# Kernel optimization log

Measured on AMD Instinct MI355X. Metric: run time of the kernel, lower is better.

Reference implementation:

```python
import jax, jax.numpy as jnp
import numpy as np

N_HEAD = 16
LN_EPS = 1e-5


def _rope_tables(T, hd, dtype):
    # Standard GPT-NeoX style rotary tables: cos/sin of shape [T, hd]
    inv = 1.0 / (10000.0 ** (np.arange(0, hd, 2, dtype=np.float64) / hd))
    freqs = np.outer(np.arange(T), inv)
    emb = np.concatenate([freqs, freqs], axis=-1)
    return jnp.asarray(np.cos(emb), dtype), jnp.asarray(np.sin(emb), dtype)


def _rotate_half(x):
    x1, x2 = jnp.split(x, 2, axis=-1)
    return jnp.concatenate([-x2, x1], axis=-1)


def _layernorm(x, g, b):
    mu = x.mean(-1, keepdims=True)
    var = x.var(-1, keepdims=True)
    return (x - mu) / jnp.sqrt(var + LN_EPS) * g + b


def _heads(x, H):
    B, T, C = x.shape
    return x.reshape(B, T, H, C // H).transpose(0, 2, 1, 3)  # [B,H,T,hd]


def _lin_attention(Q, K, V, causal):
    # Q,K,V: [B,H,T,hd]; ELU+1 feature map, RoPE on features, denom = sum_s Q.K
    Qf = jax.nn.elu(Q) + 1.0
    Kf = jax.nn.elu(K) + 1.0
    hd = Qf.shape[-1]
    cq, sq = _rope_tables(Qf.shape[2], hd, Qf.dtype)
    ck, sk = _rope_tables(Kf.shape[2], hd, Kf.dtype)
    Qr = Qf * cq + _rotate_half(Qf) * sq
    Kr = Kf * ck + _rotate_half(Kf) * sk
    # denom.sum(-1) == Qf . (sum_s Kf) -- avoid materializing a second TxS matrix
    denom = jnp.einsum('bhtd,bhd->bht', Qf, Kf.sum(axis=2))[..., None]
    att = jnp.einsum('bhtd,bhsd->bhts', Qr, Kr)
    if causal:
        T, S = att.shape[-2], att.shape[-1]
        att = jnp.where(jnp.tril(jnp.ones((T, S), dtype=bool)), att, 0.0)
    att = att / denom
    y = jnp.einsum('bhts,bhsd->bhtd', att, V)
    B, H, T, hd = y.shape
    return y.transpose(0, 2, 1, 3).reshape(B, T, H * hd)


def _forward(x, memory, ln1_g, ln1_b, sa_qkv_w, sa_qkv_b, sa_proj_w, sa_proj_b,
             ln2_g, ln2_b, ca_q_w, ca_q_b, ca_kv_w, ca_kv_b, ca_proj_w, ca_proj_b,
             ln3_g, ln3_b, fc_w, fc_b, fcp_w, fcp_b):
    H = N_HEAD
    # causal self-attention
    h = _layernorm(x, ln1_g, ln1_b)
    qkv = h @ sa_qkv_w + sa_qkv_b
    Q, K, V = jnp.split(qkv, 3, axis=-1)
    y = _lin_attention(_heads(Q, H), _heads(K, H), _heads(V, H), causal=True)
    x = x + (y @ sa_proj_w + sa_proj_b)
    # cross-attention
    h = _layernorm(x, ln2_g, ln2_b)
    q = h @ ca_q_w + ca_q_b
    kv = memory @ ca_kv_w + ca_kv_b
    K, V = jnp.split(kv, 2, axis=-1)
    y = _lin_attention(_heads(q, H), _heads(K, H), _heads(V, H), causal=False)
    x = x + (y @ ca_proj_w + ca_proj_b)
    # MLP with tanh-approx GELU
    h = _layernorm(x, ln3_g, ln3_b)
    h = jax.nn.gelu(h @ fc_w + fc_b, approximate=True)
    x = x + (h @ fcp_w + fcp_b)
    return x


def setup_inputs() -> dict:
    key = jax.random.key(0)
    ks = jax.random.split(key, 12)
    B, T, S, C = 2, 1024, 1024, 1024
    w = lambda k, shape: jax.random.normal(k, shape, dtype=jnp.float32) * 0.02
    return {
        'x': jax.random.normal(ks[0], (B, T, C), dtype=jnp.float32),
        'memory': jax.random.normal(ks[1], (B, S, C), dtype=jnp.float32),
        'ln1_g': jnp.ones((C,), jnp.float32), 'ln1_b': jnp.zeros((C,), jnp.float32),
        'sa_qkv_w': w(ks[2], (C, 3 * C)), 'sa_qkv_b': jnp.zeros((3 * C,), jnp.float32),
        'sa_proj_w': w(ks[3], (C, C)), 'sa_proj_b': jnp.zeros((C,), jnp.float32),
        'ln2_g': jnp.ones((C,), jnp.float32), 'ln2_b': jnp.zeros((C,), jnp.float32),
        'ca_q_w': w(ks[4], (C, C)), 'ca_q_b': jnp.zeros((C,), jnp.float32),
        'ca_kv_w': w(ks[5], (C, 2 * C)), 'ca_kv_b': jnp.zeros((2 * C,), jnp.float32),
        'ca_proj_w': w(ks[6], (C, C)), 'ca_proj_b': jnp.zeros((C,), jnp.float32),
        'ln3_g': jnp.ones((C,), jnp.float32), 'ln3_b': jnp.zeros((C,), jnp.float32),
        'fc_w': w(ks[7], (C, 4 * C)), 'fc_b': jnp.zeros((4 * C,), jnp.float32),
        'fcp_w': w(ks[8], (4 * C, C)), 'fcp_b': jnp.zeros((C,), jnp.float32),
    }


def reference(x, memory, ln1_g, ln1_b, sa_qkv_w, sa_qkv_b, sa_proj_w, sa_proj_b,
              ln2_g, ln2_b, ca_q_w, ca_q_b, ca_kv_w, ca_kv_b, ca_proj_w, ca_proj_b,
              ln3_g, ln3_b, fc_w, fc_b, fcp_w, fcp_b):
    return _forward(x, memory, ln1_g, ln1_b, sa_qkv_w, sa_qkv_b, sa_proj_w, sa_proj_b,
                    ln2_g, ln2_b, ca_q_w, ca_q_b, ca_kv_w, ca_kv_b, ca_proj_w, ca_proj_b,
                    ln3_g, ln3_b, fc_w, fc_b, fcp_w, fcp_b)
```

## Files before the change

kernel.cpp:

```cpp
#include <hip/hip_runtime.h>
#include <math.h>

#define BB 2
#define TT 1024
#define CC 1024
#define HH 16
#define HD 64
#define MM (BB*TT)

typedef unsigned short u16;
typedef unsigned int u32;
typedef short s16x8 __attribute__((ext_vector_type(8)));
typedef float f32x4 __attribute__((ext_vector_type(4)));

__device__ __forceinline__ u16 f2bf(float f) {
    u32 u = __builtin_bit_cast(u32, f);
    u += 0x7fffu + ((u >> 16) & 1u);
    return (u16)(u >> 16);
}
__device__ __forceinline__ float bf2f(u16 h) {
    return __builtin_bit_cast(float, ((u32)h) << 16);
}
__device__ __forceinline__ void gload16(const void* g, void* l) {
    __builtin_amdgcn_global_load_lds((const __attribute__((address_space(1))) u32*)g,
                                     (__attribute__((address_space(3))) u32*)l, 16, 0, 0);
}
__device__ __forceinline__ float gelu_tanh(float x) {
    float x3 = x * x * x;
    return 0.5f * x * (1.0f + tanhf(0.7978845608028654f * (x + 0.044715f * x3)));
}
__device__ __forceinline__ float elu1(float v) {
    return (v > 0.0f) ? v + 1.0f : expf(v);
}

__device__ __forceinline__ void wtile(const float* __restrict__ in, u16* __restrict__ out,
                                      int K, int N, int local, float (*tl)[65]) {
    int tilesX = N >> 6;
    int n0 = (local % tilesX) * 64, k0 = (local / tilesX) * 64;
    int c = threadIdx.x & 63, r4 = threadIdx.x >> 6;
    #pragma unroll
    for (int i = 0; i < 16; ++i) {
        int r = r4 * 16 + i;
        tl[r][c] = in[(size_t)(k0 + r) * N + n0 + c];
    }
    __syncthreads();
    #pragma unroll
    for (int i = 0; i < 16; ++i) {
        int r = r4 * 16 + i;
        out[(size_t)(n0 + r) * K + k0 + c] = f2bf(tl[c][r]);
    }
}

__global__ __launch_bounds__(256) void prep_kernel(
        const float* __restrict__ w_qkv, u16* __restrict__ t_qkv,
        const float* __restrict__ w_pr,  u16* __restrict__ t_pr,
        const float* __restrict__ w_caq, u16* __restrict__ t_caq,
        const float* __restrict__ w_cakv,u16* __restrict__ t_cakv,
        const float* __restrict__ w_capr,u16* __restrict__ t_capr,
        const float* __restrict__ w_fc,  u16* __restrict__ t_fc,
        const float* __restrict__ w_fcp, u16* __restrict__ t_fcp,
        const float* __restrict__ memF,  u16* __restrict__ memB,
        float* __restrict__ cosT, float* __restrict__ sinT) {
    __shared__ float tl[64][65];
    int bid = blockIdx.x;
    if (bid < 768)        wtile(w_qkv,  t_qkv,  1024, 3072, bid, tl);
    else if (bid < 1024)  wtile(w_pr,   t_pr,   1024, 1024, bid - 768, tl);
    else if (bid < 1280)  wtile(w_caq,  t_caq,  1024, 1024, bid - 1024, tl);
    else if (bid < 1792)  wtile(w_cakv, t_cakv, 1024, 2048, bid - 1280, tl);
    else if (bid < 2048)  wtile(w_capr, t_capr, 1024, 1024, bid - 1792, tl);
    else if (bid < 3072)  wtile(w_fc,   t_fc,   1024, 4096, bid - 2048, tl);
    else if (bid < 4096)  wtile(w_fcp,  t_fcp,  4096, 1024, bid - 3072, tl);
    else if (bid < 6144) {
        int i = (bid - 4096) * 256 + threadIdx.x;
        float4 v = reinterpret_cast<const float4*>(memF)[i];
        uint2 p;
        p.x = (u32)f2bf(v.x) | ((u32)f2bf(v.y) << 16);
        p.y = (u32)f2bf(v.z) | ((u32)f2bf(v.w) << 16);
        reinterpret_cast<uint2*>(memB)[i] = p;
    } else {
        int idx = (bid - 6144) * 256 + threadIdx.x;
        int t = idx >> 5, d = idx & 31;
        double inv = pow(10000.0, -((double)d) / 32.0);
        double ang = (double)t * inv;
        cosT[t * 32 + d] = (float)cos(ang);
        sinT[t * 32 + d] = (float)sin(ang);
    }
}

__global__ __launch_bounds__(256) void ln_kernel(const float* __restrict__ x,
                                                 const float* __restrict__ g,
                                                 const float* __restrict__ bta,
                                                 u16* __restrict__ out) {
    int row = blockIdx.x;
    const float* xr = x + (size_t)row * CC;
    float4 v = reinterpret_cast<const float4*>(xr)[threadIdx.x];
    float s  = v.x + v.y + v.z + v.w;
    float sq = v.x*v.x + v.y*v.y + v.z*v.z + v.w*v.w;
    #pragma unroll
    for (int off = 32; off >= 1; off >>= 1) {
        s  += __shfl_down(s, off);
        sq += __shfl_down(sq, off);
    }
    __shared__ float ls[4], lsq[4];
    int wave = threadIdx.x >> 6, lane = threadIdx.x & 63;
    if (lane == 0) { ls[wave] = s; lsq[wave] = sq; }
    __syncthreads();
    s  = ls[0] + ls[1] + ls[2] + ls[3];
    sq = lsq[0] + lsq[1] + lsq[2] + lsq[3];
    float mean = s * (1.0f / CC);
    float var  = sq * (1.0f / CC) - mean * mean;
    float rstd = rsqrtf(var + 1e-5f);
    float4 gv = reinterpret_cast<const float4*>(g)[threadIdx.x];
    float4 bv = reinterpret_cast<const float4*>(bta)[threadIdx.x];
    float o0 = (v.x - mean) * rstd * gv.x + bv.x;
    float o1 = (v.y - mean) * rstd * gv.y + bv.y;
    float o2 = (v.z - mean) * rstd * gv.z + bv.z;
    float o3 = (v.w - mean) * rstd * gv.w + bv.w;
    uint2 p;
    p.x = (u32)f2bf(o0) | ((u32)f2bf(o1) << 16);
    p.y = (u32)f2bf(o2) | ((u32)f2bf(o3) << 16);
    reinterpret_cast<uint2*>(out + (size_t)row * CC)[threadIdx.x] = p;
}

#define M_F32RES 0
#define M_GELU   1
#define M_QKV    2
#define M_PART   5
#define M_CAQKV  6

template <int MODE>
__device__ __forceinline__ void emit(int row, int col, float v,
                                     const float* __restrict__ res,
                                     float* __restrict__ oF, u16* __restrict__ o1,
                                     u16* __restrict__ o2, u16* __restrict__ o3, int N) {
    if constexpr (MODE == M_F32RES) {
        size_t o = (size_t)row * N + col;
        oF[o] = v + res[o];
    } else if constexpr (MODE == M_GELU) {
        o1[(size_t)row * N + col] = f2bf(gelu_tanh(v));
    } else {
        int b = row >> 10, t = row & 1023;
        if (col < 1024) {
            int h = col >> 6, d = col & 63;
            o1[(((size_t)(b * HH + h)) * TT + t) * HD + d] = f2bf(elu1(v));
        } else if (col < 2048) {
            int c = col - 1024, h = c >> 6, d = c & 63;
            o2[(((size_t)(b * HH + h)) * TT + t) * HD + d] = f2bf(elu1(v));
        } else {
            int c = col - 2048, h = c >> 6, d = c & 63;
            o3[(((size_t)(b * HH + h)) * HD + d) * TT + t] = f2bf(v);
        }
    }
}

template <int BM, int BN, int MODE, int SPLITK>
__global__ __launch_bounds__(512, 8) void gemm_bf16(const u16* __restrict__ A,
                                                    const u16* __restrict__ A2,
                                                    const u16* __restrict__ BT,
                                                    const u16* __restrict__ BT2,
                                                    const float* __restrict__ bias,
                                                    const float* __restrict__ bias2,
                                                    const float* __restrict__ res,
                                                    float* __restrict__ oF,
                                                    u16* __restrict__ o1,
                                                    u16* __restrict__ o2,
                                                    u16* __restrict__ o3,
                                                    float* __restrict__ ksumP,
                                                    int N, int K) {
    constexpr int WM = BM / 4, WN = BN / 2;
    constexpr int FI = WM / 16, FJ = WN / 16;
    constexpr int IA = BM * 8 / 512;
    constexpr int IB = BN * 8 / 512;
    __shared__ u16 As[BM * 64];
    __shared__ u16 Bs[BN * 64];
    int tid = threadIdx.x;
    int wave = tid >> 6, lane = tid & 63;
    int wr = wave >> 1, wc = wave & 1;
    int gx = gridDim.x, gy = gridDim.y;
    int lid = blockIdx.x + gx * blockIdx.y;
    int chunk = (gx * gy) >> 3;
    int swz = (lid & 7) * chunk + (lid >> 3);
    int bx = swz % gx, by = swz / gx;
    int row0 = by * BM, col0 = bx * BN;
    const u16* Ause = A;
    const u16* Buse = BT;
    const float* buse = bias;
    if constexpr (MODE == M_CAQKV) {
        if (col0 >= 1024) {
            Ause = A2;
            Buse = BT2 - (size_t)1024 * K;
            buse = bias2 - 1024;
        }
    }
    int kbeg = 0, kcnt = K;
    if constexpr (SPLITK > 1) { kcnt = K / SPLITK; kbeg = blockIdx.z * kcnt; }
    int kend = kbeg + kcnt;

    f32x4 acc[FI][FJ] = {};
    int lr = lane & 15;
    for (int kt = kbeg; kt < kend; kt += 64) {
        __syncthreads();
        #pragma unroll
        for (int i = 0; i < IA; ++i) {
            int s = tid + i * 512;
            int r = s >> 3, kb = s & 7;
            int kbs = kb ^ (r & 7);
            gload16(Ause + (size_t)(row0 + r) * K + kt + kbs * 8, &As[s * 8]);
        }
        #pragma unroll
        for (int i = 0; i < IB; ++i) {
            int s = tid + i * 512;
            int r = s >> 3, kb = s & 7;
            int kbs = kb ^ (r & 7);
            gload16(Buse + (size_t)(col0 + r) * K + kt + kbs * 8, &Bs[s * 8]);
        }
        __syncthreads();
        #pragma unroll
        for (int ks = 0; ks < 2; ++ks) {
            s16x8 a[FI], b[FJ];
            int kc = ks * 4 + (lane >> 4);
            int sw = (kc ^ (lr & 7)) * 8;
            #pragma unroll
            for (int i = 0; i < FI; ++i)
                a[i] = *reinterpret_cast<const s16x8*>(&As[(wr * WM + i * 16 + lr) * 64 + sw]);
            #pragma unroll
            for (int j = 0; j < FJ; ++j)
                b[j] = *reinterpret_cast<const s16x8*>(&Bs[(wc * WN + j * 16 + lr) * 64 + sw]);
            #pragma unroll
            for (int i = 0; i < FI; ++i)
                #pragma unroll
                for (int j = 0; j < FJ; ++j)
                    acc[i][j] = __builtin_amdgcn_mfma_f32_16x16x32_bf16(a[i], b[j], acc[i][j], 0, 0, 0);
        }
    }
    int lr4 = (lane >> 4) * 4;
    if constexpr (MODE == M_PART) {
        size_t zoff = (size_t)blockIdx.z * (size_t)(gridDim.y * BM) * N;
        #pragma unroll
        for (int j = 0; j < FJ; ++j) {
            int col = col0 + wc * WN + j * 16 + lr;
            #pragma unroll
            for (int i = 0; i < FI; ++i)
                #pragma unroll
                for (int r = 0; r < 4; ++r) {
                    int row = row0 + wr * WM + i * 16 + lr4 + r;
                    oF[zoff + (size_t)row * N + col] = acc[i][j][r];
                }
        }
    } else {
        constexpr int EM = (MODE == M_CAQKV) ? M_QKV : MODE;
        #pragma unroll
        for (int j = 0; j < FJ; ++j) {
            int col = col0 + wc * WN + j * 16 + lr;
            float bi = buse[col];
            #pragma unroll
            for (int i = 0; i < FI; ++i)
                #pragma unroll
                for (int r = 0; r < 4; ++r) {
                    int row = row0 + wr * WM + i * 16 + lr4 + r;
                    emit<EM>(row, col, acc[i][j][r] + bi, res, oF, o1, o2, o3, N);
                }
        }
        if constexpr (MODE == M_QKV || MODE == M_CAQKV) {
            if (col0 >= 1024 && col0 < 2048) {
                float* scratch = (float*)As;
                float part[FJ];
                #pragma unroll
                for (int j = 0; j < FJ; ++j) {
                    int col = col0 + wc * WN + j * 16 + lr;
                    float bi = buse[col];
                    float p = 0.f;
                    #pragma unroll
                    for (int i = 0; i < FI; ++i)
                        #pragma unroll
                        for (int r = 0; r < 4; ++r)
                            p += elu1(acc[i][j][r] + bi);
                    part[j] = p;
                }
                __syncthreads();
                int contrib = wr * 4 + (lane >> 4);
                #pragma unroll
                for (int j = 0; j < FJ; ++j) {
                    int colLocal = wc * WN + j * 16 + lr;
                    scratch[colLocal * 16 + contrib] = part[j];
                }
                __syncthreads();
                if (tid < BN) {
                    float s = 0.f;
                    #pragma unroll
                    for (int c = 0; c < 16; ++c) s += scratch[tid * 16 + c];
                    ksumP[(size_t)by * 1024 + (col0 - 1024) + tid] = s;
                }
            }
        }
    }
}

template <int S>
__global__ __launch_bounds__(256) void reduce_res_kernel(const float* __restrict__ P,
                                                         const float* __restrict__ bias,
                                                         const float* __restrict__ res,
                                                         float* __restrict__ out,
                                                         int N, int total4) {
    int idx = blockIdx.x * 256 + threadIdx.x;
    if (idx >= total4) return;
    float4 b = reinterpret_cast<const float4*>(bias)[idx & (N / 4 - 1)];
    float4 r = reinterpret_cast<const float4*>(res)[idx];
    float4 a = {b.x + r.x, b.y + r.y, b.z + r.z, b.w + r.w};
    #pragma unroll
    for (int s = 0; s < S; ++s) {
        float4 p = reinterpret_cast<const float4*>(P)[(size_t)s * total4 + idx];
        a.x += p.x; a.y += p.y; a.z += p.z; a.w += p.w;
    }
    reinterpret_cast<float4*>(out)[idx] = a;
}

template <int S>
__global__ __launch_bounds__(256) void reduce_ln_kernel(const float* __restrict__ P,
                                                        const float* __restrict__ bias,
                                                        const float* __restrict__ res,
                                                        const float* __restrict__ g,
                                                        const float* __restrict__ bta,
                                                        float* __restrict__ out,
                                                        u16* __restrict__ hout) {
    int row = blockIdx.x;
    int t = threadIdx.x;
    const int total4 = MM * CC / 4;
    size_t ro4 = (size_t)row * 256 + t;
    float4 b = reinterpret_cast<const float4*>(bias)[t];
    float4 r = reinterpret_cast<const float4*>(res)[ro4];
    float4 a = {b.x + r.x, b.y + r.y, b.z + r.z, b.w + r.w};
    #pragma unroll
    for (int s = 0; s < S; ++s) {
        float4 p = reinterpret_cast<const float4*>(P)[(size_t)s * total4 + ro4];
        a.x += p.x; a.y += p.y; a.z += p.z; a.w += p.w;
    }
    reinterpret_cast<float4*>(out)[ro4] = a;
    float s1 = a.x + a.y + a.z + a.w;
    float sq = a.x*a.x + a.y*a.y + a.z*a.z + a.w*a.w;
    #pragma unroll
    for (int off = 32; off >= 1; off >>= 1) {
        s1 += __shfl_down(s1, off);
        sq += __shfl_down(sq, off);
    }
    __shared__ float ls[4], lsq[4];
    int wave = t >> 6, lane = t & 63;
    if (lane == 0) { ls[wave] = s1; lsq[wave] = sq; }
    __syncthreads();
    s1 = ls[0] + ls[1] + ls[2] + ls[3];
    sq = lsq[0] + lsq[1] + lsq[2] + lsq[3];
    float mean = s1 * (1.0f / CC);
    float var  = sq * (1.0f / CC) - mean * mean;
    float rstd = rsqrtf(var + 1e-5f);
    float4 gv = reinterpret_cast<const float4*>(g)[t];
    float4 bv = reinterpret_cast<const float4*>(bta)[t];
    float o0 = (a.x - mean) * rstd * gv.x + bv.x;
    float o1 = (a.y - mean) * rstd * gv.y + bv.y;
    float o2 = (a.z - mean) * rstd * gv.z + bv.z;
    float o3 = (a.w - mean) * rstd * gv.w + bv.w;
    uint2 pk;
    pk.x = (u32)f2bf(o0) | ((u32)f2bf(o1) << 16);
    pk.y = (u32)f2bf(o2) | ((u32)f2bf(o3) << 16);
    reinterpret_cast<uint2*>(hout + (size_t)row * CC)[t] = pk;
}

__global__ __launch_bounds__(256) void denom_kernel(const u16* __restrict__ Qf,
                                                    const float* __restrict__ KsumP,
                                                    float* __restrict__ den) {
    int bh = blockIdx.x >> 5;
    int b = bh >> 4, h = bh & 15;
    int t0 = (blockIdx.x & 31) * 32;
    __shared__ float ks[64];
    if (threadIdx.x < 64) {
        float s = 0.f;
        #pragma unroll
        for (int rb = 0; rb < 8; ++rb)
            s += KsumP[(size_t)(b * 8 + rb) * 1024 + h * 64 + threadIdx.x];
        ks[threadIdx.x] = s;
    }
    __syncthreads();
    int wave = threadIdx.x >> 6, lane = threadIdx.x & 63;
    int rw = lane >> 3, lsub = lane & 7;
    int t = t0 + wave * 8 + rw;
    s16x8 q = *reinterpret_cast<const s16x8*>(&Qf[((size_t)bh * TT + t) * HD + lsub * 8]);
    float p = 0.f;
    #pragma unroll
    for (int e = 0; e < 8; ++e) p += bf2f((u16)q[e]) * ks[lsub * 8 + e];
    p += __shfl_xor(p, 1);
    p += __shfl_xor(p, 2);
    p += __shfl_xor(p, 4);
    if (lsub == 0) den[bh * TT + t] = p;
}

__global__ __launch_bounds__(256) void rope_kernel(u16* __restrict__ Qb, u16* __restrict__ Kb,
                                                   const float* __restrict__ cosT,
                                                   const float* __restrict__ sinT) {
    int g = blockIdx.x * 256 + threadIdx.x;
    u16* buf = (g & 131072) ? Kb : Qb;
    g &= 131071;
    int q = g & 3;
    int t = (g >> 2) & 1023;
    int bh = g >> 12;
    int d0 = q * 8;
    size_t base = ((size_t)bh * TT + t) * HD;
    s16x8 lo = *reinterpret_cast<const s16x8*>(&buf[base + d0]);
    s16x8 hi = *reinterpret_cast<const s16x8*>(&buf[base + 32 + d0]);
    const float4* cp = reinterpret_cast<const float4*>(&cosT[t * 32 + d0]);
    const float4* sp = reinterpret_cast<const float4*>(&sinT[t * 32 + d0]);
    float4 c0 = cp[0], c1 = cp[1], s0 = sp[0], s1 = sp[1];
    float cc[8] = {c0.x, c0.y, c0.z, c0.w, c1.x, c1.y, c1.z, c1.w};
    float ss[8] = {s0.x, s0.y, s0.z, s0.w, s1.x, s1.y, s1.z, s1.w};
    s16x8 nlo, nhi;
    #pragma unroll
    for (int e = 0; e < 8; ++e) {
        float l = bf2f((u16)lo[e]), h = bf2f((u16)hi[e]);
        nlo[e] = (short)f2bf(l * cc[e] - h * ss[e]);
        nhi[e] = (short)f2bf(h * cc[e] + l * ss[e]);
    }
    *reinterpret_cast<s16x8*>(&buf[base + d0]) = nlo;
    *reinterpret_cast<s16x8*>(&buf[base + 32 + d0]) = nhi;
}

#define APAD 72
__global__ __launch_bounds__(256) void attn_mfma(const u16* __restrict__ Qr,
                                                 const u16* __restrict__ Kr,
                                                 const u16* __restrict__ VT,
                                                 const float* __restrict__ den,
                                                 u16* __restrict__ out, int causal) {
    __shared__ u16 Qs[64 * APAD];
    __shared__ u16 Ks[64 * APAD];
    __shared__ u16 Vs[64 * APAD];
    __shared__ u16 Ps[64 * APAD];
    int lid = blockIdx.x + gridDim.x * blockIdx.y;
    int chunk = (gridDim.x * gridDim.y) >> 3;
    int swz = (lid & 7) * chunk + (lid >> 3);
    int tile = swz % gridDim.x;
    int bh = swz / gridDim.x;
    int b = bh >> 4, h = bh & 15;
    int t0 = tile * 64;
    int tid = threadIdx.x, wave = tid >> 6, lane = tid & 63;
    #pragma unroll
    for (int i = 0; i < 2; ++i) {
        int s = tid + i * 256;
        int r = s >> 3, kb = s & 7;
        *reinterpret_cast<s16x8*>(&Qs[r * APAD + kb * 8]) =
            *reinterpret_cast<const s16x8*>(&Qr[((size_t)bh * TT + t0 + r) * HD + kb * 8]);
    }
    __syncthreads();
    int lr = lane & 15, lk = (lane >> 4) * 8;
    s16x8 qf0 = *reinterpret_cast<const s16x8*>(&Qs[(wave * 16 + lr) * APAD + lk]);
    s16x8 qf1 = *reinterpret_cast<const s16x8*>(&Qs[(wave * 16 + lr) * APAD + 32 + lk]);
    f32x4 accO[4] = {};
    int ntiles = causal ? (tile + 1) : (TT / 64);
    for (int st = 0; st < ntiles; ++st) {
        int s0 = st * 64;
        __syncthreads();
        #pragma unroll
        for (int i = 0; i < 2; ++i) {
            int s = tid + i * 256;
            int r = s >> 3, kb = s & 7;
            *reinterpret_cast<s16x8*>(&Ks[r * APAD + kb * 8]) =
                *reinterpret_cast<const s16x8*>(&Kr[((size_t)bh * TT + s0 + r) * HD + kb * 8]);
            *reinterpret_cast<s16x8*>(&Vs[r * APAD + kb * 8]) =
                *reinterpret_cast<const s16x8*>(&VT[((size_t)bh * HD + r) * TT + s0 + kb * 8]);
        }
        __syncthreads();
        f32x4 accS[4] = {};
        #pragma unroll
        for (int j = 0; j < 4; ++j) {
            s16x8 kb0 = *reinterpret_cast<const s16x8*>(&Ks[(j * 16 + lr) * APAD + lk]);
            s16x8 kb1 = *reinterpret_cast<const s16x8*>(&Ks[(j * 16 + lr) * APAD + 32 + lk]);
            accS[j] = __builtin_amdgcn_mfma_f32_16x16x32_bf16(qf0, kb0, accS[j], 0, 0, 0);
            accS[j] = __builtin_amdgcn_mfma_f32_16x16x32_bf16(qf1, kb1, accS[j], 0, 0, 0);
        }
        int tl = wave * 16 + (lane >> 4) * 4;
        #pragma unroll
        for (int j = 0; j < 4; ++j) {
            #pragma unroll
            for (int r = 0; r < 4; ++r) {
                float v = accS[j][r];
                if (causal && (s0 + j * 16 + lr > t0 + tl + r)) v = 0.f;
                Ps[(tl + r) * APAD + j * 16 + lr] = f2bf(v);
            }
        }
        __syncthreads();
        #pragma unroll
        for (int ks = 0; ks < 2; ++ks) {
            s16x8 pa = *reinterpret_cast<const s16x8*>(&Ps[(wave * 16 + lr) * APAD + ks * 32 + lk]);
            #pragma unroll
            for (int j = 0; j < 4; ++j) {
                s16x8 vb = *reinterpret_cast<const s16x8*>(&Vs[(j * 16 + lr) * APAD + ks * 32 + lk]);
                accO[j] = __builtin_amdgcn_mfma_f32_16x16x32_bf16(pa, vb, accO[j], 0, 0, 0);
            }
        }
    }
    int tl = wave * 16 + (lane >> 4) * 4;
    float invd[4];
    #pragma unroll
    for (int r = 0; r < 4; ++r) invd[r] = 1.0f / den[bh * TT + t0 + tl + r];
    #pragma unroll
    for (int j = 0; j < 4; ++j)
        #pragma unroll
        for (int r = 0; r < 4; ++r)
            out[(size_t)(b * TT + t0 + tl + r) * CC + h * HD + j * 16 + lr] = f2bf(accO[j][r] * invd[r]);
}

extern "C" void kernel_launch(void* const* d_in, const int* in_sizes, int n_in,
                              void* d_out, int out_size, void* d_ws, size_t ws_size,
                              hipStream_t stream) {
    const float* x        = (const float*)d_in[0];
    const float* memory   = (const float*)d_in[1];
    const float* ln1_g    = (const float*)d_in[2];
    const float* ln1_b    = (const float*)d_in[3];
    const float* sa_qkv_w = (const float*)d_in[4];
    const float* sa_qkv_b = (const float*)d_in[5];
    const float* sa_pr_w  = (const float*)d_in[6];
    const float* sa_pr_b  = (const float*)d_in[7];
    const float* ln2_g    = (const float*)d_in[8];
    const float* ln2_b    = (const float*)d_in[9];
    const float* ca_q_w   = (const float*)d_in[10];
    const float* ca_q_b   = (const float*)d_in[11];
    const float* ca_kv_w  = (const float*)d_in[12];
    const float* ca_kv_b  = (const float*)d_in[13];
    const float* ca_pr_w  = (const float*)d_in[14];
    const float* ca_pr_b  = (const float*)d_in[15];
    const float* ln3_g    = (const float*)d_in[16];
    const float* ln3_b    = (const float*)d_in[17];
    const float* fc_w     = (const float*)d_in[18];
    const float* fc_b     = (const float*)d_in[19];
    const float* fcp_w    = (const float*)d_in[20];
    const float* fcp_b    = (const float*)d_in[21];
    float* out = (float*)d_out;
    char* wsb  = (char*)d_ws;

    const size_t MB = 1024 * 1024;
    u16* qkvT  = (u16*)wsb;
    u16* prT   = (u16*)(wsb + 6 * MB);
    u16* caqT  = (u16*)(wsb + 8 * MB);
    u16* cakvT = (u16*)(wsb + 10 * MB);
    u16* caprT = (u16*)(wsb + 14 * MB);
    u16* fcT   = (u16*)(wsb + 16 * MB);
    u16* fcpT  = (u16*)(wsb + 24 * MB);
    u16* memB  = (u16*)(wsb + 32 * MB);
    u16* hB    = (u16*)(wsb + 36 * MB);
    u16* h2B   = (u16*)(wsb + 40 * MB);
    u16* Qb    = (u16*)(wsb + 44 * MB);
    u16* Kb    = (u16*)(wsb + 48 * MB);
    u16* VTb   = (u16*)(wsb + 52 * MB);
    float* Pbuf = (float*)(wsb + 44 * MB);
    u16* fcB   = (u16*)(wsb + 60 * MB);
    float* KsumP = (float*)(wsb + 76 * MB + 65536);
    float* den   = (float*)(wsb + 76 * MB + 131072);
    float* cosT  = (float*)(wsb + 76 * MB + 262144);
    float* sinT  = (float*)(wsb + 76 * MB + 393216);

    dim3 b256(256), b512(512);
    const int TOT4 = MM * CC / 4;

    prep_kernel<<<dim3(6272), b256, 0, stream>>>(
        sa_qkv_w, qkvT, sa_pr_w, prT, ca_q_w, caqT, ca_kv_w, cakvT,
        ca_pr_w, caprT, fc_w, fcT, fcp_w, fcpT, memory, memB, cosT, sinT);

    ln_kernel<<<dim3(MM), b256, 0, stream>>>(x, ln1_g, ln1_b, hB);
    gemm_bf16<128, 64, M_QKV, 1><<<dim3(48, 16), b512, 0, stream>>>(
        hB, nullptr, qkvT, nullptr, sa_qkv_b, nullptr, nullptr,
        nullptr, Qb, Kb, VTb, KsumP, 3072, 1024);
    denom_kernel<<<dim3(1024), b256, 0, stream>>>(Qb, KsumP, den);
    rope_kernel<<<dim3(1024), b256, 0, stream>>>(Qb, Kb, cosT, sinT);
    attn_mfma<<<dim3(16, 32), b256, 0, stream>>>(Qb, Kb, VTb, den, h2B, 1);
    gemm_bf16<64, 64, M_PART, 2><<<dim3(16, 32, 2), b512, 0, stream>>>(
        h2B, nullptr, prT, nullptr, nullptr, nullptr, nullptr,
        Pbuf, nullptr, nullptr, nullptr, nullptr, 1024, 1024);
    reduce_ln_kernel<2><<<dim3(MM), b256, 0, stream>>>(Pbuf, sa_pr_b, x, ln2_g, ln2_b, out, hB);

    gemm_bf16<128, 64, M_CAQKV, 1><<<dim3(48, 16), b512, 0, stream>>>(
        hB, memB, caqT, cakvT, ca_q_b, ca_kv_b, nullptr,
        nullptr, Qb, Kb, VTb, KsumP, 3072, 1024);
    denom_kernel<<<dim3(1024), b256, 0, stream>>>(Qb, KsumP, den);
    rope_kernel<<<dim3(1024), b256, 0, stream>>>(Qb, Kb, cosT, sinT);
    attn_mfma<<<dim3(16, 32), b256, 0, stream>>>(Qb, Kb, VTb, den, h2B, 0);
    gemm_bf16<64, 64, M_PART, 2><<<dim3(16, 32, 2), b512, 0, stream>>>(
        h2B, nullptr, caprT, nullptr, nullptr, nullptr, nullptr,
        Pbuf, nullptr, nullptr, nullptr, nullptr, 1024, 1024);
    reduce_ln_kernel<2><<<dim3(MM), b256, 0, stream>>>(Pbuf, ca_pr_b, out, ln3_g, ln3_b, out, hB);

    gemm_bf16<128, 64, M_GELU, 1><<<dim3(64, 16), b512, 0, stream>>>(
        hB, nullptr, fcT, nullptr, fc_b, nullptr, nullptr,
        nullptr, fcB, nullptr, nullptr, nullptr, 4096, 1024);
    gemm_bf16<64, 64, M_PART, 2><<<dim3(16, 32, 2), b512, 0, stream>>>(
        fcB, nullptr, fcpT, nullptr, nullptr, nullptr, nullptr,
        Pbuf, nullptr, nullptr, nullptr, nullptr, 1024, 4096);
    reduce_res_kernel<2><<<dim3(TOT4 / 256), b256, 0, stream>>>(Pbuf, fcp_b, out, out, 1024, TOT4);
}
```

Before: 238.8 us.

## Fuse LN1 into prep, merge denom+rope kernels, add MFMA setprio, retile fc-proj

Folds the first layernorm into the prep kernel as extra blocks and merges the denominator and RoPE kernels into one launch. Q's RoPE runs in the same blocks after the denominator is computed, which keeps the read-before-rotate order. This removes three kernel launches and their gaps. It also wraps the MFMA sections of the GEMM and attention kernels in s_setprio to favour math waves, and switches the fc-projection split-K GEMM to 128x64 tiles, giving fewer, larger blocks.

```diff
diff --git a/kernel.cpp b/kernel.cpp
--- a/kernel.cpp
+++ b/kernel.cpp
@@ -60,7 +60,9 @@
         const float* __restrict__ w_fc,  u16* __restrict__ t_fc,
         const float* __restrict__ w_fcp, u16* __restrict__ t_fcp,
         const float* __restrict__ memF,  u16* __restrict__ memB,
-        float* __restrict__ cosT, float* __restrict__ sinT) {
+        float* __restrict__ cosT, float* __restrict__ sinT,
+        const float* __restrict__ x, const float* __restrict__ ln1_g,
+        const float* __restrict__ ln1_b, u16* __restrict__ hB) {
     __shared__ float tl[64][65];
     int bid = blockIdx.x;
     if (bid < 768)        wtile(w_qkv,  t_qkv,  1024, 3072, bid, tl);
@@ -77,49 +79,43 @@
         p.x = (u32)f2bf(v.x) | ((u32)f2bf(v.y) << 16);
         p.y = (u32)f2bf(v.z) | ((u32)f2bf(v.w) << 16);
         reinterpret_cast<uint2*>(memB)[i] = p;
-    } else {
+    } else if (bid < 6272) {
         int idx = (bid - 6144) * 256 + threadIdx.x;
         int t = idx >> 5, d = idx & 31;
         double inv = pow(10000.0, -((double)d) / 32.0);
         double ang = (double)t * inv;
         cosT[t * 32 + d] = (float)cos(ang);
         sinT[t * 32 + d] = (float)sin(ang);
-    }
-}
-
-__global__ __launch_bounds__(256) void ln_kernel(const float* __restrict__ x,
-                                                 const float* __restrict__ g,
-                                                 const float* __restrict__ bta,
-                                                 u16* __restrict__ out) {
-    int row = blockIdx.x;
-    const float* xr = x + (size_t)row * CC;
-    float4 v = reinterpret_cast<const float4*>(xr)[threadIdx.x];
-    float s  = v.x + v.y + v.z + v.w;
-    float sq = v.x*v.x + v.y*v.y + v.z*v.z + v.w*v.w;
-    #pragma unroll
-    for (int off = 32; off >= 1; off >>= 1) {
-        s  += __shfl_down(s, off);
-        sq += __shfl_down(sq, off);
-    }
-    __shared__ float ls[4], lsq[4];
-    int wave = threadIdx.x >> 6, lane = threadIdx.x & 63;
-    if (lane == 0) { ls[wave] = s; lsq[wave] = sq; }
-    __syncthreads();
-    s  = ls[0] + ls[1] + ls[2] + ls[3];
-    sq = lsq[0] + lsq[1] + lsq[2] + lsq[3];
-    float mean = s * (1.0f / CC);
-    float var  = sq * (1.0f / CC) - mean * mean;
-    float rstd = rsqrtf(var + 1e-5f);
-    float4 gv = reinterpret_cast<const float4*>(g)[threadIdx.x];
-    float4 bv = reinterpret_cast<const float4*>(bta)[threadIdx.x];
-    float o0 = (v.x - mean) * rstd * gv.x + bv.x;
-    float o1 = (v.y - mean) * rstd * gv.y + bv.y;
-    float o2 = (v.z - mean) * rstd * gv.z + bv.z;
-    float o3 = (v.w - mean) * rstd * gv.w + bv.w;
-    uint2 p;
-    p.x = (u32)f2bf(o0) | ((u32)f2bf(o1) << 16);
-    p.y = (u32)f2bf(o2) | ((u32)f2bf(o3) << 16);
-    reinterpret_cast<uint2*>(out + (size_t)row * CC)[threadIdx.x] = p;
+    } else {
+        int row = bid - 6272;
+        float4 v = reinterpret_cast<const float4*>(x + (size_t)row * CC)[threadIdx.x];
+        float s  = v.x + v.y + v.z + v.w;
+        float sq = v.x*v.x + v.y*v.y + v.z*v.z + v.w*v.w;
+        #pragma unroll
+        for (int off = 32; off >= 1; off >>= 1) {
+            s  += __shfl_down(s, off);
+            sq += __shfl_down(sq, off);
+        }
+        __shared__ float ls[4], lsq[4];
+        int wave = threadIdx.x >> 6, lane = threadIdx.x & 63;
+        if (lane == 0) { ls[wave] = s; lsq[wave] = sq; }
+        __syncthreads();
+        s  = ls[0] + ls[1] + ls[2] + ls[3];
+        sq = lsq[0] + lsq[1] + lsq[2] + lsq[3];
+        float mean = s * (1.0f / CC);
+        float var  = sq * (1.0f / CC) - mean * mean;
+        float rstd = rsqrtf(var + 1e-5f);
+        float4 gv = reinterpret_cast<const float4*>(ln1_g)[threadIdx.x];
+        float4 bv = reinterpret_cast<const float4*>(ln1_b)[threadIdx.x];
+        float o0 = (v.x - mean) * rstd * gv.x + bv.x;
+        float o1 = (v.y - mean) * rstd * gv.y + bv.y;
+        float o2 = (v.z - mean) * rstd * gv.z + bv.z;
+        float o3 = (v.w - mean) * rstd * gv.w + bv.w;
+        uint2 p;
+        p.x = (u32)f2bf(o0) | ((u32)f2bf(o1) << 16);
+        p.y = (u32)f2bf(o2) | ((u32)f2bf(o3) << 16);
+        reinterpret_cast<uint2*>(hB + (size_t)row * CC)[threadIdx.x] = p;
+    }
 }
 
 #define M_F32RES 0
@@ -226,11 +222,13 @@
             #pragma unroll
             for (int j = 0; j < FJ; ++j)
                 b[j] = *reinterpret_cast<const s16x8*>(&Bs[(wc * WN + j * 16 + lr) * 64 + sw]);
+            __builtin_amdgcn_s_setprio(1);
             #pragma unroll
             for (int i = 0; i < FI; ++i)
                 #pragma unroll
                 for (int j = 0; j < FJ; ++j)
                     acc[i][j] = __builtin_amdgcn_mfma_f32_16x16x32_bf16(a[i], b[j], acc[i][j], 0, 0, 0);
+            __builtin_amdgcn_s_setprio(0);
         }
     }
     int lr4 = (lane >> 4) * 4;
@@ -364,43 +362,9 @@
     reinterpret_cast<uint2*>(hout + (size_t)row * CC)[t] = pk;
 }
 
-__global__ __launch_bounds__(256) void denom_kernel(const u16* __restrict__ Qf,
-                                                    const float* __restrict__ KsumP,
-                                                    float* __restrict__ den) {
-    int bh = blockIdx.x >> 5;
-    int b = bh >> 4, h = bh & 15;
-    int t0 = (blockIdx.x & 31) * 32;
-    __shared__ float ks[64];
-    if (threadIdx.x < 64) {
-        float s = 0.f;
-        #pragma unroll
-        for (int rb = 0; rb < 8; ++rb)
-            s += KsumP[(size_t)(b * 8 + rb) * 1024 + h * 64 + threadIdx.x];
-        ks[threadIdx.x] = s;
-    }
-    __syncthreads();
-    int wave = threadIdx.x >> 6, lane = threadIdx.x & 63;
-    int rw = lane >> 3, lsub = lane & 7;
-    int t = t0 + wave * 8 + rw;
-    s16x8 q = *reinterpret_cast<const s16x8*>(&Qf[((size_t)bh * TT + t) * HD + lsub * 8]);
-    float p = 0.f;
-    #pragma unroll
-    for (int e = 0; e < 8; ++e) p += bf2f((u16)q[e]) * ks[lsub * 8 + e];
-    p += __shfl_xor(p, 1);
-    p += __shfl_xor(p, 2);
-    p += __shfl_xor(p, 4);
-    if (lsub == 0) den[bh * TT + t] = p;
-}
-
-__global__ __launch_bounds__(256) void rope_kernel(u16* __restrict__ Qb, u16* __restrict__ Kb,
-                                                   const float* __restrict__ cosT,
-                                                   const float* __restrict__ sinT) {
-    int g = blockIdx.x * 256 + threadIdx.x;
-    u16* buf = (g & 131072) ? Kb : Qb;
-    g &= 131071;
-    int q = g & 3;
-    int t = (g >> 2) & 1023;
-    int bh = g >> 12;
+__device__ __forceinline__ void rope_row(u16* __restrict__ buf, int bh, int t, int q,
+                                         const float* __restrict__ cosT,
+                                         const float* __restrict__ sinT) {
     int d0 = q * 8;
     size_t base = ((size_t)bh * TT + t) * HD;
     s16x8 lo = *reinterpret_cast<const s16x8*>(&buf[base + d0]);
@@ -419,6 +383,51 @@
     }
     *reinterpret_cast<s16x8*>(&buf[base + d0]) = nlo;
     *reinterpret_cast<s16x8*>(&buf[base + 32 + d0]) = nhi;
+}
+
+__global__ __launch_bounds__(256) void denom_rope_kernel(u16* __restrict__ Qb,
+                                                         u16* __restrict__ Kb,
+                                                         const float* __restrict__ KsumP,
+                                                         const float* __restrict__ cosT,
+                                                         const float* __restrict__ sinT,
+                                                         float* __restrict__ den) {
+    int bid = blockIdx.x;
+    if (bid < 1024) {
+        int bh = bid >> 5;
+        int b = bh >> 4, h = bh & 15;
+        int t0 = (bid & 31) * 32;
+        __shared__ float ks[64];
+        if (threadIdx.x < 64) {
+            float s = 0.f;
+            #pragma unroll
+            for (int rb = 0; rb < 8; ++rb)
+                s += KsumP[(size_t)(b * 8 + rb) * 1024 + h * 64 + threadIdx.x];
+            ks[threadIdx.x] = s;
+        }
+        __syncthreads();
+        int wave = threadIdx.x >> 6, lane = threadIdx.x & 63;
+        int rw = lane >> 3, lsub = lane & 7;
+        int t = t0 + wave * 8 + rw;
+        s16x8 q = *reinterpret_cast<const s16x8*>(&Qb[((size_t)bh * TT + t) * HD + lsub * 8]);
+        float p = 0.f;
+        #pragma unroll
+        for (int e = 0; e < 8; ++e) p += bf2f((u16)q[e]) * ks[lsub * 8 + e];
+        p += __shfl_xor(p, 1);
+        p += __shfl_xor(p, 2);
+        p += __shfl_xor(p, 4);
+        if (lsub == 0) den[bh * TT + t] = p;
+        __syncthreads();
+        if (threadIdx.x < 128) {
+            int row = threadIdx.x >> 2, qq = threadIdx.x & 3;
+            rope_row(Qb, bh, t0 + row, qq, cosT, sinT);
+        }
+    } else {
+        int g = (bid - 1024) * 256 + threadIdx.x;
+        int qq = g & 3;
+        int t = (g >> 2) & 1023;
+        int bh = g >> 12;
+        rope_row(Kb, bh, t, qq, cosT, sinT);
+    }
 }
 
 #define APAD 72
@@ -466,6 +475,7 @@
         }
         __syncthreads();
         f32x4 accS[4] = {};
+        __builtin_amdgcn_s_setprio(1);
         #pragma unroll
         for (int j = 0; j < 4; ++j) {
             s16x8 kb0 = *reinterpret_cast<const s16x8*>(&Ks[(j * 16 + lr) * APAD + lk]);
@@ -473,6 +483,7 @@
             accS[j] = __builtin_amdgcn_mfma_f32_16x16x32_bf16(qf0, kb0, accS[j], 0, 0, 0);
             accS[j] = __builtin_amdgcn_mfma_f32_16x16x32_bf16(qf1, kb1, accS[j], 0, 0, 0);
         }
+        __builtin_amdgcn_s_setprio(0);
         int tl = wave * 16 + (lane >> 4) * 4;
         #pragma unroll
         for (int j = 0; j < 4; ++j) {
@@ -484,6 +495,7 @@
             }
         }
         __syncthreads();
+        __builtin_amdgcn_s_setprio(1);
         #pragma unroll
         for (int ks = 0; ks < 2; ++ks) {
             s16x8 pa = *reinterpret_cast<const s16x8*>(&Ps[(wave * 16 + lr) * APAD + ks * 32 + lk]);
@@ -493,6 +505,7 @@
                 accO[j] = __builtin_amdgcn_mfma_f32_16x16x32_bf16(pa, vb, accO[j], 0, 0, 0);
             }
         }
+        __builtin_amdgcn_s_setprio(0);
     }
     int tl = wave * 16 + (lane >> 4) * 4;
     float invd[4];
@@ -557,16 +570,15 @@
     dim3 b256(256), b512(512);
     const int TOT4 = MM * CC / 4;
 
-    prep_kernel<<<dim3(6272), b256, 0, stream>>>(
+    prep_kernel<<<dim3(8320), b256, 0, stream>>>(
         sa_qkv_w, qkvT, sa_pr_w, prT, ca_q_w, caqT, ca_kv_w, cakvT,
-        ca_pr_w, caprT, fc_w, fcT, fcp_w, fcpT, memory, memB, cosT, sinT);
-
-    ln_kernel<<<dim3(MM), b256, 0, stream>>>(x, ln1_g, ln1_b, hB);
+        ca_pr_w, caprT, fc_w, fcT, fcp_w, fcpT, memory, memB, cosT, sinT,
+        x, ln1_g, ln1_b, hB);
+
     gemm_bf16<128, 64, M_QKV, 1><<<dim3(48, 16), b512, 0, stream>>>(
         hB, nullptr, qkvT, nullptr, sa_qkv_b, nullptr, nullptr,
         nullptr, Qb, Kb, VTb, KsumP, 3072, 1024);
-    denom_kernel<<<dim3(1024), b256, 0, stream>>>(Qb, KsumP, den);
-    rope_kernel<<<dim3(1024), b256, 0, stream>>>(Qb, Kb, cosT, sinT);
+    denom_rope_kernel<<<dim3(1536), b256, 0, stream>>>(Qb, Kb, KsumP, cosT, sinT, den);
     attn_mfma<<<dim3(16, 32), b256, 0, stream>>>(Qb, Kb, VTb, den, h2B, 1);
     gemm_bf16<64, 64, M_PART, 2><<<dim3(16, 32, 2), b512, 0, stream>>>(
         h2B, nullptr, prT, nullptr, nullptr, nullptr, nullptr,
@@ -576,8 +588,7 @@
     gemm_bf16<128, 64, M_CAQKV, 1><<<dim3(48, 16), b512, 0, stream>>>(
         hB, memB, caqT, cakvT, ca_q_b, ca_kv_b, nullptr,
         nullptr, Qb, Kb, VTb, KsumP, 3072, 1024);
-    denom_kernel<<<dim3(1024), b256, 0, stream>>>(Qb, KsumP, den);
-    rope_kernel<<<dim3(1024), b256, 0, stream>>>(Qb, Kb, cosT, sinT);
+    denom_rope_kernel<<<dim3(1536), b256, 0, stream>>>(Qb, Kb, KsumP, cosT, sinT, den);
     attn_mfma<<<dim3(16, 32), b256, 0, stream>>>(Qb, Kb, VTb, den, h2B, 0);
     gemm_bf16<64, 64, M_PART, 2><<<dim3(16, 32, 2), b512, 0, stream>>>(
         h2B, nullptr, caprT, nullptr, nullptr, nullptr, nullptr,
@@ -587,7 +598,7 @@
     gemm_bf16<128, 64, M_GELU, 1><<<dim3(64, 16), b512, 0, stream>>>(
         hB, nullptr, fcT, nullptr, fc_b, nullptr, nullptr,
         nullptr, fcB, nullptr, nullptr, nullptr, 4096, 1024);
-    gemm_bf16<64, 64, M_PART, 2><<<dim3(16, 32, 2), b512, 0, stream>>>(
+    gemm_bf16<128, 64, M_PART, 2><<<dim3(16, 16, 2), b512, 0, stream>>>(
         fcB, nullptr, fcpT, nullptr, nullptr, nullptr, nullptr,
         Pbuf, nullptr, nullptr, nullptr, nullptr, 1024, 4096);
     reduce_res_kernel<2><<<dim3(TOT4 / 256), b256, 0, stream>>>(Pbuf, fcp_b, out, out, 1024, TOT4);
```

After: 232.3 us. 2.8% less time.
